# Optimization experiments

Measured on AMD Instinct MI355X. Metric: run time of the kernel, lower is better.

The kernel has to match this reference:

```python
import jax, jax.numpy as jnp
import numpy as np

B, N, F, G, H = 8, 1024, 512, 128, 8
D = F // H  # head_dim = 64


def setup_inputs() -> dict:
    key = jax.random.key(0)
    ks = jax.random.split(key, 24)
    def lin(k, fan_in, shape):
        return jax.random.normal(k, shape, jnp.float32) / np.sqrt(fan_in)
    return {
        "features": jax.random.normal(ks[0], (B, N, F), jnp.float32),
        "geometry": jax.random.normal(ks[1], (B, N, G), jnp.float32),
        "coords": jax.random.normal(ks[2], (B, N, 3), jnp.float32),
        # nnx.MultiHeadAttention params (q/k/v/out dense, with bias)
        "wq": lin(ks[3], F, (F, F)), "bq": jnp.zeros((F,), jnp.float32),
        "wk": lin(ks[4], F, (F, F)), "bk": jnp.zeros((F,), jnp.float32),
        "wv": lin(ks[5], F, (F, F)), "bv": jnp.zeros((F,), jnp.float32),
        "wo": lin(ks[6], F, (F, F)), "bo": jnp.zeros((F,), jnp.float32),
        # geometry q/k/v linears
        "gq_w": lin(ks[7], G, (G, F)), "gq_b": jnp.zeros((F,), jnp.float32),
        "gk_w": lin(ks[8], G, (G, F)), "gk_b": jnp.zeros((F,), jnp.float32),
        "gv_w": lin(ks[9], G, (G, F)), "gv_b": jnp.zeros((F,), jnp.float32),
        # distance MLP: Linear(1->H), gelu, Linear(H->H)
        "d1_w": lin(ks[10], 1, (1, H)), "d1_b": jnp.zeros((H,), jnp.float32),
        "d2_w": lin(ks[11], H, (H, H)), "d2_b": jnp.zeros((H,), jnp.float32),
        # output projection
        "op_w": lin(ks[12], F, (F, F)), "op_b": jnp.zeros((F,), jnp.float32),
    }


def _forward(features, geometry, coords,
             wq, bq, wk, bk, wv, bv, wo, bo,
             gq_w, gq_b, gk_w, gk_b, gv_w, gv_b,
             d1_w, d1_b, d2_w, d2_b, op_w, op_b):
    scale = jnp.sqrt(jnp.float32(D))
    # --- standard multi-head self-attention branch (nnx.MultiHeadAttention) ---
    q = (features @ wq + bq).reshape(B, N, H, D)
    k = (features @ wk + bk).reshape(B, N, H, D)
    v = (features @ wv + bv).reshape(B, N, H, D)
    scores = jnp.einsum("bqhd,bkhd->bhqk", q, k) / scale
    attn = jax.nn.softmax(scores, axis=-1)
    feat_att = jnp.einsum("bhqk,bkhd->bqhd", attn, v).reshape(B, N, F)
    feat_att = feat_att @ wo + bo
    # --- geometry attention branch ---
    gq = geometry @ gq_w + gq_b
    gk = geometry @ gk_w + gk_b
    gv = geometry @ gv_w + gv_b
    g_scores = jnp.einsum("bqd,bkd->bqk", gq, gk) / scale
    # pairwise distances (B,N,N,1); clamp for sqrt-at-zero safety (diagonal)
    diff = coords[:, :, None, :] - coords[:, None, :, :]
    dist = jnp.sqrt(jnp.maximum(jnp.sum(diff * diff, -1, keepdims=True), 1e-12))
    dw = jax.nn.gelu(dist @ d1_w + d1_b) @ d2_w + d2_b  # (B,N,N,H)
    # transpose to (B,H,N,N) then mean over heads == mean over last axis
    g_scores = g_scores + jnp.mean(dw, axis=-1)
    g_attn = jax.nn.softmax(g_scores, axis=-1)
    geom_att = jnp.einsum("bqk,bkd->bqd", g_attn, gv)
    return (feat_att + geom_att) @ op_w + op_b


def reference(features, geometry, coords,
              wq, bq, wk, bk, wv, bv, wo, bo,
              gq_w, gq_b, gk_w, gk_b, gv_w, gv_b,
              d1_w, d1_b, d2_w, d2_b, op_w, op_b):
    return _forward(features, geometry, coords,
                    wq, bq, wk, bk, wv, bv, wo, bo,
                    gq_w, gq_b, gk_w, gk_b, gv_w, gv_b,
                    d1_w, d1_b, d2_w, d2_b, op_w, op_b)
```

## Files before the change

kernel.cpp:

```cpp
#include <hip/hip_runtime.h>

typedef __bf16 bf16_t;
typedef __bf16 bf16x8 __attribute__((ext_vector_type(8)));
typedef __bf16 bf16x4v __attribute__((ext_vector_type(4)));
typedef float f32x4 __attribute__((ext_vector_type(4)));

#define MFMA16(a, b, c) __builtin_amdgcn_mfma_f32_16x16x32_bf16((a), (b), (c), 0, 0, 0)

static constexpr int B_ = 8, N_ = 1024, F_ = 512, H_ = 8;
static constexpr int M_ = B_ * N_;
static constexpr float LOG2E = 1.4426950408889634f;

__device__ __forceinline__ void gl_lds16(const bf16_t* gsrc, bf16_t* ldst) {
  __builtin_amdgcn_global_load_lds(
      (const __attribute__((address_space(1))) void*)gsrc,
      (__attribute__((address_space(3))) void*)ldst, 16, 0, 0);
}

__device__ __forceinline__ float gelu_tanh(float u) {
  float g = 0.7978845608028654f * fmaf(0.044715f * u * u, u, u);
  float e = __expf(2.f * g);
  float t = 1.f - 2.f / (e + 1.f);
  return 0.5f * u * (1.f + t);
}

struct PrepArgs {
  const float *features, *geometry;
  const float *wq, *wk, *wv, *wo, *op_w;
  const float *gq_w, *gk_w, *gv_w;
  const float *bq, *bk, *bv, *gq_b, *gk_b, *gv_b;
  const float *d1w, *d1b, *d2w, *d2b;
  bf16_t *featBF, *geomBF, *WqkvT, *GqkvT, *WoT, *OpT;
  float *bqkv, *gqkvb, *dlut;
};

static constexpr int PR_C0 = 4096;
static constexpr int PR_C1 = PR_C0 + 1024;
static constexpr int PR_WQ = PR_C1 + 256;
static constexpr int PR_WK = PR_WQ + 256;
static constexpr int PR_WV = PR_WK + 256;
static constexpr int PR_WO = PR_WV + 256;
static constexpr int PR_OP = PR_WO + 256;
static constexpr int PR_GQ = PR_OP + 64;
static constexpr int PR_GK = PR_GQ + 64;
static constexpr int PR_GV = PR_GK + 64;
static constexpr int PR_B1 = PR_GV + 6;
static constexpr int PR_B2 = PR_B1 + 6;
static constexpr int PR_LUT = PR_B2 + 16;
static constexpr int PR_TOTAL = PR_LUT;

__device__ __forceinline__ void prep_cast(const float* __restrict__ in,
                                          bf16_t* __restrict__ out, int blk) {
  int i = blk * 256 + threadIdx.x;
  float4 v = ((const float4*)in)[i];
  bf16x4v o;
  o[0] = (bf16_t)v.x; o[1] = (bf16_t)v.y; o[2] = (bf16_t)v.z; o[3] = (bf16_t)v.w;
  ((bf16x4v*)out)[i] = o;
}

__device__ __forceinline__ void prep_transpose(const float* __restrict__ W,
                                               bf16_t* __restrict__ Wt,
                                               int K, int N, int ldo, int idx,
                                               float (*t)[33]) {
  const int bx = idx & 15, by = idx >> 4;
  const int kb = by * 32, cb = bx * 32;
  const int tx = threadIdx.x & 31, ty = threadIdx.x >> 5;
#pragma unroll
  for (int i = 0; i < 4; ++i)
    t[ty * 4 + i][tx] = W[(long)(kb + ty * 4 + i) * N + cb + tx];
  __syncthreads();
#pragma unroll
  for (int i = 0; i < 4; ++i)
    Wt[(long)(cb + ty * 4 + i) * ldo + kb + tx] = (bf16_t)t[tx][ty * 4 + i];
}

__global__ __launch_bounds__(256) void k_prep(PrepArgs p) {
  __shared__ float tsh[32][33];
  const int blk = blockIdx.x;
  if (blk < PR_C0) {
    prep_cast(p.features, p.featBF, blk);
  } else if (blk < PR_C1) {
    prep_cast(p.geometry, p.geomBF, blk - PR_C0);
  } else if (blk < PR_WQ) {
    prep_transpose(p.wq, p.WqkvT, 512, 512, 512, blk - PR_C1, tsh);
  } else if (blk < PR_WK) {
    prep_transpose(p.wk, p.WqkvT + 512 * 512, 512, 512, 512, blk - PR_WQ, tsh);
  } else if (blk < PR_WV) {
    prep_transpose(p.wv, p.WqkvT + 1024 * 512, 512, 512, 512, blk - PR_WK, tsh);
  } else if (blk < PR_WO) {
    prep_transpose(p.wo, p.WoT, 512, 512, 512, blk - PR_WV, tsh);
  } else if (blk < PR_OP) {
    prep_transpose(p.op_w, p.OpT, 512, 512, 512, blk - PR_WO, tsh);
  } else if (blk < PR_GQ) {
    prep_transpose(p.gq_w, p.GqkvT, 128, 512, 128, blk - PR_OP, tsh);
  } else if (blk < PR_GK) {
    prep_transpose(p.gk_w, p.GqkvT + 512 * 128, 128, 512, 128, blk - PR_GQ, tsh);
  } else if (blk < PR_GV) {
    prep_transpose(p.gv_w, p.GqkvT + 1024 * 128, 128, 512, 128, blk - PR_GK, tsh);
  } else if (blk < PR_B1) {
    int i = (blk - PR_GV) * 256 + threadIdx.x;
    p.bqkv[i] = i < 512 ? p.bq[i] : (i < 1024 ? p.bk[i - 512] : p.bv[i - 1024]);
  } else if (blk < PR_B2) {
    int i = (blk - PR_B1) * 256 + threadIdx.x;
    p.gqkvb[i] = i < 512 ? p.gq_b[i] : (i < 1024 ? p.gk_b[i - 512] : p.gv_b[i - 1024]);
  } else {
    int i = (blk - PR_B2) * 256 + threadIdx.x;
    float d = (i + 0.5f) * (16.f / 4096.f);
    float s = 0.f;
#pragma unroll
    for (int h = 0; h < 8; ++h) s += p.d2b[h];
    s *= 0.125f;
#pragma unroll
    for (int j = 0; j < 8; ++j) {
      float w2 = 0.f;
#pragma unroll
      for (int h = 0; h < 8; ++h) w2 += p.d2w[j * 8 + h];
      s = fmaf(gelu_tanh(fmaf(d, p.d1w[j], p.d1b[j])), w2 * 0.125f, s);
    }
    p.dlut[i] = s;
  }
}

struct GemmArgs {
  const bf16_t* A; const bf16_t* Bt;
  const float* bias; const float* addSrc; const bf16_t* addSrcB;
  const float* coords; const float* lut;
  float* outF; bf16_t* outB;
  bf16_t* outT;
  long strideAb; long strideBb;
  int lda, ldb, K, ldout;
  float scale;
};

__device__ __forceinline__ void gemm128_core(const GemmArgs& g, int mBase, int cBase,
                                             bf16_t (*As)[64], bf16_t (*Bs)[64]) {
  const int tid = threadIdx.x;
  const int w = tid >> 6, lane = tid & 63;
  const int lr = lane & 15, lg = lane >> 4;
  const int wr = w >> 1, wc = w & 1;
  const int batch = mBase >> 10;

  const int srow = lane >> 3;
  const int scol = (lane & 7) * 8;
  const bf16_t* Ag = g.A + (long)batch * g.strideAb +
                     (long)((mBase & 1023) + w * 32 + srow) * g.lda + scol;
  const bf16_t* Bg = g.Bt + (long)batch * g.strideBb +
                     (long)(cBase + w * 32 + srow) * g.ldb + scol;
  bf16_t* Al = &As[w * 32][0];
  bf16_t* Bl = &Bs[w * 32][0];

  f32x4 zero = {0.f, 0.f, 0.f, 0.f};
  f32x4 acc[4][4];
#pragma unroll
  for (int i = 0; i < 4; ++i)
#pragma unroll
    for (int j = 0; j < 4; ++j) acc[i][j] = zero;

  for (int k0 = 0; k0 < g.K; k0 += 64) {
#pragma unroll
    for (int is = 0; is < 4; ++is) {
      gl_lds16(Ag + (long)(is * 8) * g.lda + k0, Al + is * 8 * 64);
      gl_lds16(Bg + (long)(is * 8) * g.ldb + k0, Bl + is * 8 * 64);
    }
    __syncthreads();
#pragma unroll
    for (int ks = 0; ks < 2; ++ks) {
      bf16x8 a[4], b[4];
#pragma unroll
      for (int i = 0; i < 4; ++i) {
        a[i] = *(const bf16x8*)(&As[wr * 64 + i * 16 + lr][ks * 32 + lg * 8]);
        b[i] = *(const bf16x8*)(&Bs[wc * 64 + i * 16 + lr][ks * 32 + lg * 8]);
      }
#pragma unroll
      for (int mf = 0; mf < 4; ++mf)
#pragma unroll
        for (int nf = 0; nf < 4; ++nf)
          acc[mf][nf] = MFMA16(a[mf], b[nf], acc[mf][nf]);
    }
    __syncthreads();
  }

  const int c0 = cBase + wc * 64;
  float bias4[4];
#pragma unroll
  for (int nf = 0; nf < 4; ++nf)
    bias4[nf] = g.bias ? g.bias[c0 + nf * 16 + lr] : 0.f;
  const bool vtile = (g.outT != nullptr) && (cBase >= 1024);
#pragma unroll
  for (int mf = 0; mf < 4; ++mf) {
    const int r0 = mBase + wr * 64 + mf * 16 + lg * 4;
    const int r0b = r0 & 1023;
#pragma unroll
    for (int nf = 0; nf < 4; ++nf) {
      const int c = c0 + nf * 16 + lr;
      if (vtile) {
        bf16x4v vv;
#pragma unroll
        for (int rg = 0; rg < 4; ++rg)
          vv[rg] = (bf16_t)(acc[mf][nf][rg] * g.scale + bias4[nf]);
        *(bf16x4v*)(&g.outT[((long)batch * 512 + (c - 1024)) * 1024 + r0b]) = vv;
      } else {
#pragma unroll
        for (int rg = 0; rg < 4; ++rg) {
          const int r = r0 + rg;
          float v = acc[mf][nf][rg] * g.scale + bias4[nf];
          if (g.addSrc) v += g.addSrc[(long)r * g.ldout + c];
          const long oi = (long)r * g.ldout + c;
          if (g.outF) g.outF[oi] = v;
          if (g.outB) g.outB[oi] = (bf16_t)v;
        }
      }
    }
  }
}

__global__ __launch_bounds__(256) void k_gemm128_dual(GemmArgs g1, GemmArgs g2) {
  __shared__ alignas(16) bf16_t As[128][64];
  __shared__ alignas(16) bf16_t Bs[128][64];
  const int y = blockIdx.y;
  if (y < 64) gemm128_core(g1, y * 128, blockIdx.x * 128, As, Bs);
  else        gemm128_core(g2, (y - 64) * 128, blockIdx.x * 128, As, Bs);
}

__device__ __forceinline__ void gemm128_dist(const GemmArgs& g, int mBase, int cBase,
                                             char* smemc) {
  bf16_t (*As)[64] = (bf16_t (*)[64])smemc;
  bf16_t (*Bs)[64] = (bf16_t (*)[64])(smemc + 16384);
  bf16_t* Lut = (bf16_t*)(smemc + 32768);
  const int tid = threadIdx.x;
  const int w = tid >> 6, lane = tid & 63;
  const int lr = lane & 15, lg = lane >> 4;
  const int wr = w >> 1, wc = w & 1;
  const int batch = mBase >> 10;

  {
    const float4* src = (const float4*)g.lut;
#pragma unroll
    for (int i = 0; i < 4; ++i) {
      float4 v = src[tid + i * 256];
      bf16x4v o;
      o[0] = (bf16_t)(v.x * LOG2E); o[1] = (bf16_t)(v.y * LOG2E);
      o[2] = (bf16_t)(v.z * LOG2E); o[3] = (bf16_t)(v.w * LOG2E);
      ((bf16x4v*)Lut)[tid + i * 256] = o;
    }
  }

  const int srow = lane >> 3;
  const int scol = (lane & 7) * 8;
  const bf16_t* Ag = g.A + (long)batch * g.strideAb +
                     (long)((mBase & 1023) + w * 32 + srow) * g.lda + scol;
  const bf16_t* Bg = g.Bt + (long)batch * g.strideBb +
                     (long)(cBase + w * 32 + srow) * g.ldb + scol;
  bf16_t* Al = &As[w * 32][0];
  bf16_t* Bl = &Bs[w * 32][0];

  f32x4 zero = {0.f, 0.f, 0.f, 0.f};
  f32x4 acc[4][4];
#pragma unroll
  for (int i = 0; i < 4; ++i)
#pragma unroll
    for (int j = 0; j < 4; ++j) acc[i][j] = zero;

  for (int k0 = 0; k0 < g.K; k0 += 64) {
#pragma unroll
    for (int is = 0; is < 4; ++is) {
      gl_lds16(Ag + (long)(is * 8) * g.lda + k0, Al + is * 8 * 64);
      gl_lds16(Bg + (long)(is * 8) * g.ldb + k0, Bl + is * 8 * 64);
    }
    __syncthreads();
#pragma unroll
    for (int ks = 0; ks < 2; ++ks) {
      bf16x8 a[4], b[4];
#pragma unroll
      for (int i = 0; i < 4; ++i) {
        a[i] = *(const bf16x8*)(&As[wr * 64 + i * 16 + lr][ks * 32 + lg * 8]);
        b[i] = *(const bf16x8*)(&Bs[wc * 64 + i * 16 + lr][ks * 32 + lg * 8]);
      }
#pragma unroll
      for (int mf = 0; mf < 4; ++mf)
#pragma unroll
        for (int nf = 0; nf < 4; ++nf)
          acc[mf][nf] = MFMA16(a[mf], b[nf], acc[mf][nf]);
    }
    __syncthreads();
  }

  const int c0 = cBase + wc * 64;
  float ckx[4], cky[4], ckz[4];
#pragma unroll
  for (int nf = 0; nf < 4; ++nf) {
    const float* ck = g.coords + ((long)batch * 1024 + c0 + nf * 16 + lr) * 3;
    ckx[nf] = ck[0]; cky[nf] = ck[1]; ckz[nf] = ck[2];
  }
#pragma unroll
  for (int mf = 0; mf < 4; ++mf) {
    const int r0 = mBase + wr * 64 + mf * 16 + lg * 4;
    float cqx[4], cqy[4], cqz[4];
#pragma unroll
    for (int rg = 0; rg < 4; ++rg) {
      const float* cq = g.coords + ((long)batch * 1024 + ((r0 + rg) & 1023)) * 3;
      cqx[rg] = cq[0]; cqy[rg] = cq[1]; cqz[rg] = cq[2];
    }
#pragma unroll
    for (int nf = 0; nf < 4; ++nf) {
      const int c = c0 + nf * 16 + lr;
#pragma unroll
      for (int rg = 0; rg < 4; ++rg) {
        const int r = r0 + rg;
        float v = acc[mf][nf][rg] * g.scale;
        float dx = cqx[rg] - ckx[nf], dy = cqy[rg] - cky[nf], dz = cqz[rg] - ckz[nf];
        float d = sqrtf(fmaxf(dx * dx + dy * dy + dz * dz, 1e-12f));
        int idx = (int)(d * 256.f);
        idx = idx > 4095 ? 4095 : idx;
        g.outB[(long)r * g.ldout + c] = (bf16_t)exp2f(v + (float)Lut[idx]);
      }
    }
  }
}

__device__ __forceinline__ void flash_core(const bf16_t* __restrict__ QKV,
                                           const bf16_t* __restrict__ Vt,
                                           bf16_t* __restrict__ fatt,
                                           int qx, int bh, char* smemc) {
  bf16_t (*Ks)[64][64] = (bf16_t (*)[64][64])smemc;
  bf16_t (*Vs)[64][64] = (bf16_t (*)[64][64])(smemc + 16384);
  char* Plb = smemc + 32768;
  const int wave = threadIdx.x >> 6, lane = threadIdx.x & 63;
  const int lr = lane & 15, lg = (lane >> 4) & 3;
  const int b = bh >> 3, h = bh & 7;
  const int qbase = qx * 64 + wave * 16;

  const bf16_t* Qb = QKV + (long)b * 1024 * 1536 + h * 64;
  const bf16_t* Kb = Qb + 512;
  const bf16_t* Vg = Vt + ((long)b * 512 + h * 64) * 1024;

  constexpr float SCL = 0.18033688011112042f;
  bf16x8 q_[2];
#pragma unroll
  for (int dh = 0; dh < 2; ++dh) {
    bf16x8 raw = *(const bf16x8*)(Qb + (long)(qbase + lr) * 1536 + dh * 32 + lg * 8);
#pragma unroll
    for (int j = 0; j < 8; ++j) q_[dh][j] = (bf16_t)((float)raw[j] * SCL);
  }
  bf16x8 onesb;
#pragma unroll
  for (int j = 0; j < 8; ++j) onesb[j] = (bf16_t)1.0f;

  const int srow = lane >> 3;
  const int scol = (((lane & 7) ^ srow) << 3);
  const bf16_t* KgB = Kb + (long)(wave * 16 + srow) * 1536 + scol;
  const bf16_t* VgB = Vg + (long)(wave * 16 + srow) * 1024 + scol;

  auto stage = [&](int buf, int kt) {
#pragma unroll
    for (int i = 0; i < 2; ++i) {
      gl_lds16(KgB + (long)(kt + i * 8) * 1536, &Ks[buf][wave * 16 + i * 8][0]);
      gl_lds16(VgB + (long)(i * 8) * 1024 + kt, &Vs[buf][wave * 16 + i * 8][0]);
    }
  };

  f32x4 zero = {0.f, 0.f, 0.f, 0.f};
  f32x4 oacc[4] = {zero, zero, zero, zero};
  f32x4 oL = zero;
  const int swz = (lr & 7) << 4;
  char* PlW = Plb + wave * 1280;

  stage(0, 0);
  asm volatile("s_waitcnt vmcnt(0)" ::: "memory");
  __syncthreads();

  auto tile = [&](const int buf, int t) __attribute__((always_inline)) {
    if (t < 15) stage(buf ^ 1, (t + 1) * 64);
    const char* KB = (const char*)&Ks[buf][0][0];
    const char* VB = (const char*)&Vs[buf][0][0];
#pragma unroll
    for (int kk = 0; kk < 2; ++kk) {
      f32x4 S[2];
      __builtin_amdgcn_s_setprio(1);
#pragma unroll
      for (int kh = 0; kh < 2; ++kh) {
        const int row = kk * 32 + kh * 16 + lr;
        bf16x8 k0 = *(const bf16x8*)(KB + row * 128 + ((lg * 16) ^ swz));
        bf16x8 k1 = *(const bf16x8*)(KB + row * 128 + ((64 + lg * 16) ^ swz));
        f32x4 tt = MFMA16(k0, q_[0], zero);
        S[kh] = MFMA16(k1, q_[1], tt);
      }
      __builtin_amdgcn_s_setprio(0);
#pragma unroll
      for (int kh = 0; kh < 2; ++kh) {
        bf16x4v pp;
#pragma unroll
        for (int r = 0; r < 4; ++r) pp[r] = (bf16_t)exp2f(S[kh][r]);
        *(bf16x4v*)(PlW + lr * 80 + kh * 32 + lg * 8) = pp;
      }
      asm volatile("s_waitcnt lgkmcnt(0)" ::: "memory");
      const bf16x8 pa = *(const bf16x8*)(PlW + lr * 80 + lg * 16);
      __builtin_amdgcn_s_setprio(1);
#pragma unroll
      for (int ct = 0; ct < 4; ++ct) {
        const int vrow = ct * 16 + lr;
        bf16x8 vf = *(const bf16x8*)(VB + vrow * 128 + ((kk * 64 + lg * 16) ^ swz));
        oacc[ct] = MFMA16(pa, vf, oacc[ct]);
      }
      oL = MFMA16(pa, onesb, oL);
      __builtin_amdgcn_s_setprio(0);
    }
    asm volatile("s_waitcnt vmcnt(0)" ::: "memory");
    __syncthreads();
  };

  for (int tt = 0; tt < 8; ++tt) {
    tile(0, tt * 2);
    tile(1, tt * 2 + 1);
  }

#pragma unroll
  for (int r = 0; r < 4; ++r) {
    float inv = 1.f / oL[r];
    int q = qbase + lg * 4 + r;
    bf16_t* orow = fatt + ((long)b * 1024 + q) * 512 + h * 64;
#pragma unroll
    for (int ct = 0; ct < 4; ++ct)
      orow[ct * 16 + lr] = (bf16_t)(oacc[ct][r] * inv);
  }
}

__global__ __launch_bounds__(256) void k_gsc_flash(GemmArgs g,
                                                   const bf16_t* __restrict__ QKV,
                                                   const bf16_t* __restrict__ Vt,
                                                   bf16_t* __restrict__ fatt) {
  __shared__ alignas(16) char smem[40960];
  const int bx = blockIdx.x;
  if (bx < 512) {
    gemm128_dist(g, (bx >> 3) * 128, (bx & 7) * 128, smem);
  } else {
    const int fid = bx - 512;
    flash_core(QKV, Vt, fatt, fid & 15, fid >> 4, smem);
  }
}

template <int RSUM>
__global__ __launch_bounds__(256) void k_gemm_n64(GemmArgs g) {
  __shared__ alignas(16) bf16_t As[128][64];
  __shared__ alignas(16) bf16_t Bs[64][64];
  const int tid = threadIdx.x;
  const int w = tid >> 6, lane = tid & 63;
  const int lr = lane & 15, lg = lane >> 4;
  const int wr = w >> 1, wc = w & 1;
  const int mBase = blockIdx.y * 128, cBase = blockIdx.x * 64;
  const int batch = mBase >> 10;

  const int srow = lane >> 3;
  const int scol = (lane & 7) * 8;
  const bf16_t* Ag = g.A + (long)batch * g.strideAb +
                     (long)((mBase & 1023) + w * 32 + srow) * g.lda + scol;
  const bf16_t* Bg = g.Bt + (long)batch * g.strideBb +
                     (long)(cBase + w * 16 + srow) * g.ldb + scol;
  bf16_t* Al = &As[w * 32][0];
  bf16_t* Bl = &Bs[w * 16][0];

  f32x4 zero = {0.f, 0.f, 0.f, 0.f};
  f32x4 acc[4][2];
#pragma unroll
  for (int i = 0; i < 4; ++i)
#pragma unroll
    for (int j = 0; j < 2; ++j) acc[i][j] = zero;
  f32x4 lacc[4] = {zero, zero, zero, zero};
  bf16x8 onesb;
#pragma unroll
  for (int j = 0; j < 8; ++j) onesb[j] = (bf16_t)1.0f;

  for (int k0 = 0; k0 < g.K; k0 += 64) {
#pragma unroll
    for (int is = 0; is < 4; ++is)
      gl_lds16(Ag + (long)(is * 8) * g.lda + k0, Al + is * 8 * 64);
#pragma unroll
    for (int is = 0; is < 2; ++is)
      gl_lds16(Bg + (long)(is * 8) * g.ldb + k0, Bl + is * 8 * 64);
    __syncthreads();
#pragma unroll
    for (int ks = 0; ks < 2; ++ks) {
      bf16x8 a[4], b[2];
#pragma unroll
      for (int i = 0; i < 4; ++i)
        a[i] = *(const bf16x8*)(&As[wr * 64 + i * 16 + lr][ks * 32 + lg * 8]);
#pragma unroll
      for (int j = 0; j < 2; ++j)
        b[j] = *(const bf16x8*)(&Bs[wc * 32 + j * 16 + lr][ks * 32 + lg * 8]);
#pragma unroll
      for (int mf = 0; mf < 4; ++mf)
#pragma unroll
        for (int nf = 0; nf < 2; ++nf)
          acc[mf][nf] = MFMA16(a[mf], b[nf], acc[mf][nf]);
      if constexpr (RSUM) {
#pragma unroll
        for (int mf = 0; mf < 4; ++mf)
          lacc[mf] = MFMA16(a[mf], onesb, lacc[mf]);
      }
    }
    __syncthreads();
  }

  const int c0 = cBase + wc * 32;
  float bias2[2];
#pragma unroll
  for (int nf = 0; nf < 2; ++nf)
    bias2[nf] = g.bias ? g.bias[c0 + nf * 16 + lr] : 0.f;
#pragma unroll
  for (int mf = 0; mf < 4; ++mf) {
    const int r0 = mBase + wr * 64 + mf * 16 + lg * 4;
    float linv[4];
    if constexpr (RSUM) {
#pragma unroll
      for (int rg = 0; rg < 4; ++rg) linv[rg] = 1.f / lacc[mf][rg];
    }
#pragma unroll
    for (int nf = 0; nf < 2; ++nf) {
      const int c = c0 + nf * 16 + lr;
#pragma unroll
      for (int rg = 0; rg < 4; ++rg) {
        const int r = r0 + rg;
        float v = acc[mf][nf][rg] * g.scale + bias2[nf];
        if constexpr (RSUM) v *= linv[rg];
        const long oi = (long)r * g.ldout + c;
        if (g.addSrc) v += g.addSrc[oi];
        if (g.addSrcB) v += (float)g.addSrcB[oi];
        if (g.outF) g.outF[oi] = v;
        if (g.outB) g.outB[oi] = (bf16_t)v;
      }
    }
  }
}

extern "C" void kernel_launch(void* const* d_in, const int* in_sizes, int n_in,
                              void* d_out, int out_size, void* d_ws, size_t ws_size,
                              hipStream_t stream) {
  const float* features = (const float*)d_in[0];
  const float* geometry = (const float*)d_in[1];
  const float* coords   = (const float*)d_in[2];
  const float* wq = (const float*)d_in[3];  const float* bq = (const float*)d_in[4];
  const float* wk = (const float*)d_in[5];  const float* bk = (const float*)d_in[6];
  const float* wv = (const float*)d_in[7];  const float* bv = (const float*)d_in[8];
  const float* wo = (const float*)d_in[9];  const float* bo = (const float*)d_in[10];
  const float* gq_w = (const float*)d_in[11]; const float* gq_b = (const float*)d_in[12];
  const float* gk_w = (const float*)d_in[13]; const float* gk_b = (const float*)d_in[14];
  const float* gv_w = (const float*)d_in[15]; const float* gv_b = (const float*)d_in[16];
  const float* d1_w = (const float*)d_in[17]; const float* d1_b = (const float*)d_in[18];
  const float* d2_w = (const float*)d_in[19]; const float* d2_b = (const float*)d_in[20];
  const float* op_w = (const float*)d_in[21]; const float* op_b = (const float*)d_in[22];

  size_t off = 0;
  auto carve = [&](size_t bytes) {
    void* p = (char*)d_ws + off;
    off += (bytes + 255) & ~(size_t)255;
    return p;
  };
  bf16_t* featBF = (bf16_t*)carve((size_t)M_ * F_ * 2);
  bf16_t* geomBF = (bf16_t*)carve((size_t)M_ * 128 * 2);
  bf16_t* WqkvT  = (bf16_t*)carve((size_t)1536 * 512 * 2);
  bf16_t* GqkvT  = (bf16_t*)carve((size_t)1536 * 128 * 2);
  bf16_t* WoT    = (bf16_t*)carve((size_t)512 * 512 * 2);
  bf16_t* OpT    = (bf16_t*)carve((size_t)512 * 512 * 2);
  float*  bqkv   = (float*)carve(1536 * 4);
  float*  gqkvb  = (float*)carve(1536 * 4);
  float*  dlut   = (float*)carve(4096 * 4);
  bf16_t* QKV    = (bf16_t*)carve((size_t)M_ * 1536 * 2);
  bf16_t* GQKV   = (bf16_t*)carve((size_t)M_ * 1536 * 2);
  bf16_t* Vt     = (bf16_t*)carve((size_t)B_ * 512 * 1024 * 2);
  bf16_t* GVt    = (bf16_t*)carve((size_t)B_ * 512 * 1024 * 2);
  bf16_t* Pun    = (bf16_t*)carve((size_t)M_ * 1024 * 2);
  bf16_t* fatt   = (bf16_t*)carve((size_t)M_ * 512 * 2);
  bf16_t* combFb = (bf16_t*)carve((size_t)M_ * 512 * 2);
  bf16_t* combB  = (bf16_t*)carve((size_t)M_ * 512 * 2);
  if (off > ws_size) return;

  PrepArgs p;
  p.features = features; p.geometry = geometry;
  p.wq = wq; p.wk = wk; p.wv = wv; p.wo = wo; p.op_w = op_w;
  p.gq_w = gq_w; p.gk_w = gk_w; p.gv_w = gv_w;
  p.bq = bq; p.bk = bk; p.bv = bv; p.gq_b = gq_b; p.gk_b = gk_b; p.gv_b = gv_b;
  p.d1w = d1_w; p.d1b = d1_b; p.d2w = d2_w; p.d2b = d2_b;
  p.featBF = featBF; p.geomBF = geomBF; p.WqkvT = WqkvT; p.GqkvT = GqkvT;
  p.WoT = WoT; p.OpT = OpT; p.bqkv = bqkv; p.gqkvb = gqkvb; p.dlut = dlut;
  k_prep<<<PR_TOTAL, 256, 0, stream>>>(p);

  auto mk = [](const bf16_t* A, long sAb, int lda, const bf16_t* Bt, long sBb, int ldb,
               int K, const float* bias, const float* addSrc, const bf16_t* addSrcB,
               float* outF, bf16_t* outB, int ldout, float scale,
               const float* coords, const float* lut, bf16_t* outT) {
    GemmArgs g;
    g.A = A; g.Bt = Bt; g.bias = bias; g.addSrc = addSrc; g.addSrcB = addSrcB;
    g.coords = coords; g.lut = lut; g.outF = outF; g.outB = outB; g.outT = outT;
    g.strideAb = sAb; g.strideBb = sBb; g.lda = lda; g.ldb = ldb;
    g.K = K; g.ldout = ldout; g.scale = scale;
    return g;
  };

  k_gemm128_dual<<<dim3(12, 128), 256, 0, stream>>>(
      mk(featBF, (long)1024 * 512, 512, WqkvT, 0, 512, 512,
         bqkv, nullptr, nullptr, nullptr, QKV, 1536, 1.f, nullptr, nullptr, Vt),
      mk(geomBF, (long)1024 * 128, 128, GqkvT, 0, 128, 128,
         gqkvb, nullptr, nullptr, nullptr, GQKV, 1536, 1.f, nullptr, nullptr, GVt));
  k_gsc_flash<<<1536, 256, 0, stream>>>(
      mk(GQKV, (long)1024 * 1536, 1536, GQKV + 512, (long)1024 * 1536, 1536, 512,
         nullptr, nullptr, nullptr, nullptr, Pun, 1024, 0.125f * LOG2E,
         coords, dlut, nullptr),
      QKV, Vt, fatt);
  k_gemm_n64<0><<<dim3(8, 64), 256, 0, stream>>>(
      mk(fatt, (long)1024 * 512, 512, WoT, 0, 512, 512,
         bo, nullptr, nullptr, nullptr, combFb, 512, 1.f, nullptr, nullptr, nullptr));
  k_gemm_n64<1><<<dim3(8, 64), 256, 0, stream>>>(
      mk(Pun, (long)1024 * 1024, 1024, GVt, (long)512 * 1024, 1024, 1024,
         nullptr, nullptr, combFb, nullptr, combB, 512, 1.f, nullptr, nullptr, nullptr));
  k_gemm_n64<0><<<dim3(8, 64), 256, 0, stream>>>(
      mk(combB, (long)1024 * 512, 512, OpT, 0, 512, 512,
         op_b, nullptr, nullptr, (float*)d_out, nullptr, 512, 1.f, nullptr, nullptr, nullptr));
}
```

Measured before the change: 186.7 us.

## Merge Wo and geometry-PV GEMMs into one launch, sum inputs in final GEMM

The output-projection GEMM (fatt·Wo) and the geometry attention-value GEMM (Pun·GVt) are independent. They now run as two halves of a single 1024-block launch instead of two dependent launches, which removes one kernel boundary and raises the block count per launch. The residual add moves out of the second GEMM's epilogue. The final GEMM now sums the two bf16 intermediates while staging A into LDS, using register loads in place of direct global-to-LDS loads. That adds VALU work and an extra bf16 rounding in the final GEMM's A path.

Result: slower. 198.8 us (+6.4%).

```diff
diff --git a/kernel.cpp b/kernel.cpp
--- a/kernel.cpp
+++ b/kernel.cpp
@@ -122,7 +122,7 @@
 }
 
 struct GemmArgs {
-  const bf16_t* A; const bf16_t* Bt;
+  const bf16_t* A; const bf16_t* A2; const bf16_t* Bt;
   const float* bias; const float* addSrc; const bf16_t* addSrcB;
   const float* coords; const float* lut;
   float* outF; bf16_t* outB;
@@ -439,21 +439,20 @@
   }
 }
 
-template <int RSUM>
-__global__ __launch_bounds__(256) void k_gemm_n64(GemmArgs g) {
-  __shared__ alignas(16) bf16_t As[128][64];
-  __shared__ alignas(16) bf16_t Bs[64][64];
+template <int RSUM, int SUMA>
+__device__ __forceinline__ void gemm_n64_core(const GemmArgs& g, int mBase, int cBase,
+                                              bf16_t (*As)[64], bf16_t (*Bs)[64]) {
   const int tid = threadIdx.x;
   const int w = tid >> 6, lane = tid & 63;
   const int lr = lane & 15, lg = lane >> 4;
   const int wr = w >> 1, wc = w & 1;
-  const int mBase = blockIdx.y * 128, cBase = blockIdx.x * 64;
   const int batch = mBase >> 10;
 
   const int srow = lane >> 3;
   const int scol = (lane & 7) * 8;
   const bf16_t* Ag = g.A + (long)batch * g.strideAb +
                      (long)((mBase & 1023) + w * 32 + srow) * g.lda + scol;
+  const bf16_t* Ag2 = SUMA ? g.A2 + (Ag - g.A) : nullptr;
   const bf16_t* Bg = g.Bt + (long)batch * g.strideBb +
                      (long)(cBase + w * 16 + srow) * g.ldb + scol;
   bf16_t* Al = &As[w * 32][0];
@@ -471,9 +470,21 @@
   for (int j = 0; j < 8; ++j) onesb[j] = (bf16_t)1.0f;
 
   for (int k0 = 0; k0 < g.K; k0 += 64) {
-#pragma unroll
-    for (int is = 0; is < 4; ++is)
-      gl_lds16(Ag + (long)(is * 8) * g.lda + k0, Al + is * 8 * 64);
+    if constexpr (SUMA) {
+#pragma unroll
+      for (int is = 0; is < 4; ++is) {
+        bf16x8 a1 = *(const bf16x8*)(Ag + (long)(is * 8) * g.lda + k0);
+        bf16x8 a2 = *(const bf16x8*)(Ag2 + (long)(is * 8) * g.lda + k0);
+        bf16x8 s;
+#pragma unroll
+        for (int j = 0; j < 8; ++j) s[j] = (bf16_t)((float)a1[j] + (float)a2[j]);
+        *(bf16x8*)(&As[w * 32 + is * 8 + srow][scol]) = s;
+      }
+    } else {
+#pragma unroll
+      for (int is = 0; is < 4; ++is)
+        gl_lds16(Ag + (long)(is * 8) * g.lda + k0, Al + is * 8 * 64);
+    }
 #pragma unroll
     for (int is = 0; is < 2; ++is)
       gl_lds16(Bg + (long)(is * 8) * g.ldb + k0, Bl + is * 8 * 64);
@@ -530,6 +541,24 @@
       }
     }
   }
+}
+
+__global__ __launch_bounds__(256) void k_dual_n64(GemmArgs gF, GemmArgs gG) {
+  __shared__ alignas(16) bf16_t As[128][64];
+  __shared__ alignas(16) bf16_t Bs[64][64];
+  const int bx = blockIdx.x;
+  if (bx < 512) {
+    gemm_n64_core<0, 0>(gF, (bx >> 3) * 128, (bx & 7) * 64, As, Bs);
+  } else {
+    const int i = bx - 512;
+    gemm_n64_core<1, 0>(gG, (i >> 3) * 128, (i & 7) * 64, As, Bs);
+  }
+}
+
+__global__ __launch_bounds__(256) void k_final_n64(GemmArgs g) {
+  __shared__ alignas(16) bf16_t As[128][64];
+  __shared__ alignas(16) bf16_t Bs[64][64];
+  gemm_n64_core<0, 1>(g, blockIdx.y * 128, blockIdx.x * 64, As, Bs);
 }
 
 extern "C" void kernel_launch(void* const* d_in, const int* in_sizes, int n_in,
@@ -571,7 +600,7 @@
   bf16_t* Pun    = (bf16_t*)carve((size_t)M_ * 1024 * 2);
   bf16_t* fatt   = (bf16_t*)carve((size_t)M_ * 512 * 2);
   bf16_t* combFb = (bf16_t*)carve((size_t)M_ * 512 * 2);
-  bf16_t* combB  = (bf16_t*)carve((size_t)M_ * 512 * 2);
+  bf16_t* geoatt = (bf16_t*)carve((size_t)M_ * 512 * 2);
   if (off > ws_size) return;
 
   PrepArgs p;
@@ -584,35 +613,37 @@
   p.WoT = WoT; p.OpT = OpT; p.bqkv = bqkv; p.gqkvb = gqkvb; p.dlut = dlut;
   k_prep<<<PR_TOTAL, 256, 0, stream>>>(p);
 
-  auto mk = [](const bf16_t* A, long sAb, int lda, const bf16_t* Bt, long sBb, int ldb,
-               int K, const float* bias, const float* addSrc, const bf16_t* addSrcB,
+  auto mk = [](const bf16_t* A, const bf16_t* A2, long sAb, int lda,
+               const bf16_t* Bt, long sBb, int ldb, int K,
+               const float* bias, const float* addSrc, const bf16_t* addSrcB,
                float* outF, bf16_t* outB, int ldout, float scale,
                const float* coords, const float* lut, bf16_t* outT) {
     GemmArgs g;
-    g.A = A; g.Bt = Bt; g.bias = bias; g.addSrc = addSrc; g.addSrcB = addSrcB;
-    g.coords = coords; g.lut = lut; g.outF = outF; g.outB = outB; g.outT = outT;
+    g.A = A; g.A2 = A2; g.Bt = Bt; g.bias = bias; g.addSrc = addSrc;
+    g.addSrcB = addSrcB; g.coords = coords; g.lut = lut;
+    g.outF = outF; g.outB = outB; g.outT = outT;
     g.strideAb = sAb; g.strideBb = sBb; g.lda = lda; g.ldb = ldb;
     g.K = K; g.ldout = ldout; g.scale = scale;
     return g;
   };
 
   k_gemm128_dual<<<dim3(12, 128), 256, 0, stream>>>(
-      mk(featBF, (long)1024 * 512, 512, WqkvT, 0, 512, 512,
+      mk(featBF, nullptr, (long)1024 * 512, 512, WqkvT, 0, 512, 512,
          bqkv, nullptr, nullptr, nullptr, QKV, 1536, 1.f, nullptr, nullptr, Vt),
-      mk(geomBF, (long)1024 * 128, 128, GqkvT, 0, 128, 128,
+      mk(geomBF, nullptr, (long)1024 * 128, 128, GqkvT, 0, 128, 128,
          gqkvb, nullptr, nullptr, nullptr, GQKV, 1536, 1.f, nullptr, nullptr, GVt));
   k_gsc_flash<<<1536, 256, 0, stream>>>(
-      mk(GQKV, (long)1024 * 1536, 1536, GQKV + 512, (long)1024 * 1536, 1536, 512,
-         nullptr, nullptr, nullptr, nullptr, Pun, 1024, 0.125f * LOG2E,
+      mk(GQKV, nullptr, (long)1024 * 1536, 1536, GQKV + 512, (long)1024 * 1536, 1536,
+         512, nullptr, nullptr, nullptr, nullptr, Pun, 1024, 0.125f * LOG2E,
          coords, dlut, nullptr),
       QKV, Vt, fatt);
-  k_gemm_n64<0><<<dim3(8, 64), 256, 0, stream>>>(
-      mk(fatt, (long)1024 * 512, 512, WoT, 0, 512, 512,
-         bo, nullptr, nullptr, nullptr, combFb, 512, 1.f, nullptr, nullptr, nullptr));
-  k_gemm_n64<1><<<dim3(8, 64), 256, 0, stream>>>(
-      mk(Pun, (long)1024 * 1024, 1024, GVt, (long)512 * 1024, 1024, 1024,
-         nullptr, nullptr, combFb, nullptr, combB, 512, 1.f, nullptr, nullptr, nullptr));
-  k_gemm_n64<0><<<dim3(8, 64), 256, 0, stream>>>(
-      mk(combB, (long)1024 * 512, 512, OpT, 0, 512, 512,
-         op_b, nullptr, nullptr, (float*)d_out, nullptr, 512, 1.f, nullptr, nullptr, nullptr));
-}
+  k_dual_n64<<<1024, 256, 0, stream>>>(
+      mk(fatt, nullptr, (long)1024 * 512, 512, WoT, 0, 512, 512,
+         bo, nullptr, nullptr, nullptr, combFb, 512, 1.f, nullptr, nullptr, nullptr),
+      mk(Pun, nullptr, (long)1024 * 1024, 1024, GVt, (long)512 * 1024, 1024, 1024,
+         nullptr, nullptr, nullptr, nullptr, geoatt, 512, 1.f, nullptr, nullptr, nullptr));
+  k_final_n64<<<dim3(8, 64), 256, 0, stream>>>(
+      mk(combFb, geoatt, (long)1024 * 512, 512, OpT, 0, 512, 512,
+         op_b, nullptr, nullptr, (float*)d_out, nullptr, 512, 1.f,
+         nullptr, nullptr, nullptr));
+}
```

## Reassociate geometry scores as (gq·Gkᵀ)·geometryᵀ to shrink the K dimension

Applied to the files above, without the earlier changes.

Rewrites the geometry score computation gq·gkᵀ as (gq·gk_wᵀ)·geometryᵀ. A small GEMM produces an effective 128-wide query, so the flash score kernel contracts over 128 instead of 512 and the gk projection is no longer computed. gk_b is dropped, which is valid because a key bias adds a per-row constant to the scores and the softmax cancels it. The dual projection kernel now uses a flattened 1D grid with fewer geometry tiles. This adds an extra kernel launch and an extra bf16 rounding step on the intermediate query.

New measurement: 184.4 us. Within noise of the previous version (-1.2%).

```diff
diff --git a/kernel.cpp b/kernel.cpp
--- a/kernel.cpp
+++ b/kernel.cpp
@@ -28,24 +28,24 @@
   const float *features, *geometry;
   const float *wq, *wk, *wv, *wo, *op_w;
   const float *gq_w, *gk_w, *gv_w;
-  const float *bq, *bk, *bv, *gq_b, *gk_b, *gv_b;
+  const float *bq, *bk, *bv, *gq_b, *gv_b;
   const float *d1w, *d1b, *d2w, *d2b;
-  bf16_t *featBF, *geomBF, *WqkvT, *GqkvT, *WoT, *OpT;
-  float *bqkv, *gqkvb, *dlut;
+  bf16_t *featBF, *geomBF, *gkwBF, *WqkvT, *GqvT, *WoT, *OpT;
+  float *bqkv, *gqvb, *dlut;
 };
 
 static constexpr int PR_C0 = 4096;
 static constexpr int PR_C1 = PR_C0 + 1024;
-static constexpr int PR_WQ = PR_C1 + 256;
+static constexpr int PR_GKC = PR_C1 + 64;
+static constexpr int PR_WQ = PR_GKC + 256;
 static constexpr int PR_WK = PR_WQ + 256;
 static constexpr int PR_WV = PR_WK + 256;
 static constexpr int PR_WO = PR_WV + 256;
 static constexpr int PR_OP = PR_WO + 256;
 static constexpr int PR_GQ = PR_OP + 64;
-static constexpr int PR_GK = PR_GQ + 64;
-static constexpr int PR_GV = PR_GK + 64;
+static constexpr int PR_GV = PR_GQ + 64;
 static constexpr int PR_B1 = PR_GV + 6;
-static constexpr int PR_B2 = PR_B1 + 6;
+static constexpr int PR_B2 = PR_B1 + 4;
 static constexpr int PR_LUT = PR_B2 + 16;
 static constexpr int PR_TOTAL = PR_LUT;
 
@@ -81,8 +81,10 @@
     prep_cast(p.features, p.featBF, blk);
   } else if (blk < PR_C1) {
     prep_cast(p.geometry, p.geomBF, blk - PR_C0);
+  } else if (blk < PR_GKC) {
+    prep_cast(p.gk_w, p.gkwBF, blk - PR_C1);
   } else if (blk < PR_WQ) {
-    prep_transpose(p.wq, p.WqkvT, 512, 512, 512, blk - PR_C1, tsh);
+    prep_transpose(p.wq, p.WqkvT, 512, 512, 512, blk - PR_GKC, tsh);
   } else if (blk < PR_WK) {
     prep_transpose(p.wk, p.WqkvT + 512 * 512, 512, 512, 512, blk - PR_WQ, tsh);
   } else if (blk < PR_WV) {
@@ -92,17 +94,15 @@
   } else if (blk < PR_OP) {
     prep_transpose(p.op_w, p.OpT, 512, 512, 512, blk - PR_WO, tsh);
   } else if (blk < PR_GQ) {
-    prep_transpose(p.gq_w, p.GqkvT, 128, 512, 128, blk - PR_OP, tsh);
-  } else if (blk < PR_GK) {
-    prep_transpose(p.gk_w, p.GqkvT + 512 * 128, 128, 512, 128, blk - PR_GQ, tsh);
+    prep_transpose(p.gq_w, p.GqvT, 128, 512, 128, blk - PR_OP, tsh);
   } else if (blk < PR_GV) {
-    prep_transpose(p.gv_w, p.GqkvT + 1024 * 128, 128, 512, 128, blk - PR_GK, tsh);
+    prep_transpose(p.gv_w, p.GqvT + 512 * 128, 128, 512, 128, blk - PR_GQ, tsh);
   } else if (blk < PR_B1) {
     int i = (blk - PR_GV) * 256 + threadIdx.x;
     p.bqkv[i] = i < 512 ? p.bq[i] : (i < 1024 ? p.bk[i - 512] : p.bv[i - 1024]);
   } else if (blk < PR_B2) {
     int i = (blk - PR_B1) * 256 + threadIdx.x;
-    p.gqkvb[i] = i < 512 ? p.gq_b[i] : (i < 1024 ? p.gk_b[i - 512] : p.gv_b[i - 1024]);
+    p.gqvb[i] = i < 512 ? p.gq_b[i] : p.gv_b[i - 512];
   } else {
     int i = (blk - PR_B2) * 256 + threadIdx.x;
     float d = (i + 0.5f) * (16.f / 4096.f);
@@ -127,6 +127,7 @@
   const float* coords; const float* lut;
   float* outF; bf16_t* outB;
   bf16_t* outT;
+  int vtileFrom;
   long strideAb; long strideBb;
   int lda, ldb, K, ldout;
   float scale;
@@ -185,7 +186,7 @@
 #pragma unroll
   for (int nf = 0; nf < 4; ++nf)
     bias4[nf] = g.bias ? g.bias[c0 + nf * 16 + lr] : 0.f;
-  const bool vtile = (g.outT != nullptr) && (cBase >= 1024);
+  const bool vtile = (g.outT != nullptr) && (cBase >= g.vtileFrom);
 #pragma unroll
   for (int mf = 0; mf < 4; ++mf) {
     const int r0 = mBase + wr * 64 + mf * 16 + lg * 4;
@@ -198,7 +199,7 @@
 #pragma unroll
         for (int rg = 0; rg < 4; ++rg)
           vv[rg] = (bf16_t)(acc[mf][nf][rg] * g.scale + bias4[nf]);
-        *(bf16x4v*)(&g.outT[((long)batch * 512 + (c - 1024)) * 1024 + r0b]) = vv;
+        *(bf16x4v*)(&g.outT[((long)batch * 512 + (c - g.vtileFrom)) * 1024 + r0b]) = vv;
       } else {
 #pragma unroll
         for (int rg = 0; rg < 4; ++rg) {
@@ -217,9 +218,13 @@
 __global__ __launch_bounds__(256) void k_gemm128_dual(GemmArgs g1, GemmArgs g2) {
   __shared__ alignas(16) bf16_t As[128][64];
   __shared__ alignas(16) bf16_t Bs[128][64];
-  const int y = blockIdx.y;
-  if (y < 64) gemm128_core(g1, y * 128, blockIdx.x * 128, As, Bs);
-  else        gemm128_core(g2, (y - 64) * 128, blockIdx.x * 128, As, Bs);
+  const int bx = blockIdx.x;
+  if (bx < 768) {
+    gemm128_core(g1, (bx / 12) * 128, (bx % 12) * 128, As, Bs);
+  } else {
+    const int i = bx - 768;
+    gemm128_core(g2, (i / 8) * 128, (i % 8) * 128, As, Bs);
+  }
 }
 
 __device__ __forceinline__ void gemm128_dist(const GemmArgs& g, int mBase, int cBase,
@@ -548,6 +553,7 @@
   const float* d1_w = (const float*)d_in[17]; const float* d1_b = (const float*)d_in[18];
   const float* d2_w = (const float*)d_in[19]; const float* d2_b = (const float*)d_in[20];
   const float* op_w = (const float*)d_in[21]; const float* op_b = (const float*)d_in[22];
+  (void)gk_b;
 
   size_t off = 0;
   auto carve = [&](size_t bytes) {
@@ -557,15 +563,17 @@
   };
   bf16_t* featBF = (bf16_t*)carve((size_t)M_ * F_ * 2);
   bf16_t* geomBF = (bf16_t*)carve((size_t)M_ * 128 * 2);
+  bf16_t* gkwBF  = (bf16_t*)carve((size_t)128 * 512 * 2);
   bf16_t* WqkvT  = (bf16_t*)carve((size_t)1536 * 512 * 2);
-  bf16_t* GqkvT  = (bf16_t*)carve((size_t)1536 * 128 * 2);
+  bf16_t* GqvT   = (bf16_t*)carve((size_t)1024 * 128 * 2);
   bf16_t* WoT    = (bf16_t*)carve((size_t)512 * 512 * 2);
   bf16_t* OpT    = (bf16_t*)carve((size_t)512 * 512 * 2);
   float*  bqkv   = (float*)carve(1536 * 4);
-  float*  gqkvb  = (float*)carve(1536 * 4);
+  float*  gqvb   = (float*)carve(1024 * 4);
   float*  dlut   = (float*)carve(4096 * 4);
   bf16_t* QKV    = (bf16_t*)carve((size_t)M_ * 1536 * 2);
-  bf16_t* GQKV   = (bf16_t*)carve((size_t)M_ * 1536 * 2);
+  bf16_t* GQV    = (bf16_t*)carve((size_t)M_ * 1024 * 2);
+  bf16_t* GQeff  = (bf16_t*)carve((size_t)M_ * 128 * 2);
   bf16_t* Vt     = (bf16_t*)carve((size_t)B_ * 512 * 1024 * 2);
   bf16_t* GVt    = (bf16_t*)carve((size_t)B_ * 512 * 1024 * 2);
   bf16_t* Pun    = (bf16_t*)carve((size_t)M_ * 1024 * 2);
@@ -578,41 +586,50 @@
   p.features = features; p.geometry = geometry;
   p.wq = wq; p.wk = wk; p.wv = wv; p.wo = wo; p.op_w = op_w;
   p.gq_w = gq_w; p.gk_w = gk_w; p.gv_w = gv_w;
-  p.bq = bq; p.bk = bk; p.bv = bv; p.gq_b = gq_b; p.gk_b = gk_b; p.gv_b = gv_b;
+  p.bq = bq; p.bk = bk; p.bv = bv; p.gq_b = gq_b; p.gv_b = gv_b;
   p.d1w = d1_w; p.d1b = d1_b; p.d2w = d2_w; p.d2b = d2_b;
-  p.featBF = featBF; p.geomBF = geomBF; p.WqkvT = WqkvT; p.GqkvT = GqkvT;
-  p.WoT = WoT; p.OpT = OpT; p.bqkv = bqkv; p.gqkvb = gqkvb; p.dlut = dlut;
+  p.featBF = featBF; p.geomBF = geomBF; p.gkwBF = gkwBF; p.WqkvT = WqkvT;
+  p.GqvT = GqvT; p.WoT = WoT; p.OpT = OpT;
+  p.bqkv = bqkv; p.gqvb = gqvb; p.dlut = dlut;
   k_prep<<<PR_TOTAL, 256, 0, stream>>>(p);
 
   auto mk = [](const bf16_t* A, long sAb, int lda, const bf16_t* Bt, long sBb, int ldb,
                int K, const float* bias, const float* addSrc, const bf16_t* addSrcB,
                float* outF, bf16_t* outB, int ldout, float scale,
-               const float* coords, const float* lut, bf16_t* outT) {
+               const float* coords, const float* lut, bf16_t* outT, int vtileFrom) {
     GemmArgs g;
     g.A = A; g.Bt = Bt; g.bias = bias; g.addSrc = addSrc; g.addSrcB = addSrcB;
     g.coords = coords; g.lut = lut; g.outF = outF; g.outB = outB; g.outT = outT;
+    g.vtileFrom = vtileFrom;
     g.strideAb = sAb; g.strideBb = sBb; g.lda = lda; g.ldb = ldb;
     g.K = K; g.ldout = ldout; g.scale = scale;
     return g;
   };
 
-  k_gemm128_dual<<<dim3(12, 128), 256, 0, stream>>>(
+  k_gemm128_dual<<<1280, 256, 0, stream>>>(
       mk(featBF, (long)1024 * 512, 512, WqkvT, 0, 512, 512,
-         bqkv, nullptr, nullptr, nullptr, QKV, 1536, 1.f, nullptr, nullptr, Vt),
-      mk(geomBF, (long)1024 * 128, 128, GqkvT, 0, 128, 128,
-         gqkvb, nullptr, nullptr, nullptr, GQKV, 1536, 1.f, nullptr, nullptr, GVt));
+         bqkv, nullptr, nullptr, nullptr, QKV, 1536, 1.f, nullptr, nullptr, Vt, 1024),
+      mk(geomBF, (long)1024 * 128, 128, GqvT, 0, 128, 128,
+         gqvb, nullptr, nullptr, nullptr, GQV, 1024, 1.f, nullptr, nullptr, GVt, 512));
+  k_gemm_n64<0><<<dim3(2, 64), 256, 0, stream>>>(
+      mk(GQV, (long)1024 * 1024, 1024, gkwBF, 0, 512, 512,
+         nullptr, nullptr, nullptr, nullptr, GQeff, 128, 1.f, nullptr, nullptr,
+         nullptr, 1 << 30));
   k_gsc_flash<<<1536, 256, 0, stream>>>(
-      mk(GQKV, (long)1024 * 1536, 1536, GQKV + 512, (long)1024 * 1536, 1536, 512,
+      mk(GQeff, (long)1024 * 128, 128, geomBF, (long)1024 * 128, 128, 128,
          nullptr, nullptr, nullptr, nullptr, Pun, 1024, 0.125f * LOG2E,
-         coords, dlut, nullptr),
+         coords, dlut, nullptr, 1 << 30),
       QKV, Vt, fatt);
   k_gemm_n64<0><<<dim3(8, 64), 256, 0, stream>>>(
       mk(fatt, (long)1024 * 512, 512, WoT, 0, 512, 512,
-         bo, nullptr, nullptr, nullptr, combFb, 512, 1.f, nullptr, nullptr, nullptr));
+         bo, nullptr, nullptr, nullptr, combFb, 512, 1.f, nullptr, nullptr,
+         nullptr, 1 << 30));
   k_gemm_n64<1><<<dim3(8, 64), 256, 0, stream>>>(
       mk(Pun, (long)1024 * 1024, 1024, GVt, (long)512 * 1024, 1024, 1024,
-         nullptr, nullptr, combFb, nullptr, combB, 512, 1.f, nullptr, nullptr, nullptr));
+         nullptr, nullptr, combFb, nullptr, combB, 512, 1.f, nullptr, nullptr,
+         nullptr, 1 << 30));
   k_gemm_n64<0><<<dim3(8, 64), 256, 0, stream>>>(
       mk(combB, (long)1024 * 512, 512, OpT, 0, 512, 512,
-         op_b, nullptr, nullptr, (float*)d_out, nullptr, 512, 1.f, nullptr, nullptr, nullptr));
-}
+         op_b, nullptr, nullptr, (float*)d_out, nullptr, 512, 1.f, nullptr, nullptr,
+         nullptr, 1 << 30));
+}
```
